# Optimization experiments

Measured on AMD Instinct MI355X. Metric: run time of the kernel, lower is better.

## Reference

```python
import jax, jax.numpy as jnp
import numpy as np
from jax import lax

DIM = 192
HEADS = 6
WIDTH = 256
HEIGHT = 128
BATCH = 2


def _conv1x1(x, w):
    # x: [b,c,h,w], w: [o,c] (1x1 conv, no bias)
    return jnp.einsum('bchw,oc->bohw', x, w)


def setup_inputs() -> dict:
    key = jax.random.key(0)
    ks = jax.random.split(key, 7)
    c = DIM
    std = c ** -0.5
    x = jax.random.normal(ks[0], (BATCH, c, HEIGHT, WIDTH), dtype=jnp.float32)
    rpb_table = 0.02 * jax.random.normal(ks[1], (2 * WIDTH - 1, HEADS), dtype=jnp.float32)
    w_qkv = std * jax.random.normal(ks[2], (3 * c, c), dtype=jnp.float32)
    w_depth = (1.0 / 3.0) * jax.random.normal(ks[3], (3 * c, 1, 3, 3), dtype=jnp.float32)
    w_pre = std * jax.random.normal(ks[4], (c, c), dtype=jnp.float32)
    w_out = std * jax.random.normal(ks[5], (c, c), dtype=jnp.float32)
    w_gate = std * jax.random.normal(ks[6], (c, c), dtype=jnp.float32)
    return {"x": x, "rpb_table": rpb_table, "w_qkv": w_qkv, "w_depth": w_depth,
            "w_pre": w_pre, "w_out": w_out, "w_gate": w_gate, "num_heads": HEADS}


def reference(x, rpb_table, w_qkv, w_depth, w_pre, w_out, w_gate, num_heads):
    b, c, h, w = x.shape
    hd = c // num_heads
    scale = hd ** -0.5

    x_gate = jax.nn.silu(_conv1x1(x, w_gate))

    t = _conv1x1(x, w_qkv)  # [b, 3c, h, w]
    qkv = lax.conv_general_dilated(
        t, w_depth, window_strides=(1, 1), padding='SAME',
        feature_group_count=3 * c,
        dimension_numbers=('NCHW', 'OIHW', 'NCHW'))
    q, k, v = jnp.split(qkv, 3, axis=1)

    def _rows(z):
        # 'b (head c) h w -> b h head w c'
        return z.reshape(b, num_heads, hd, h, w).transpose(0, 3, 1, 4, 2)

    q = _rows(q) * scale
    k = _rows(k)
    v = _rows(v)

    attn = jnp.einsum('bhnic,bhnjc->bhnij', q, k)  # [b, h, heads, w, w]

    # relative position bias: index[i, j] = i - j + (w - 1)
    idx = jnp.arange(w)[:, None] - jnp.arange(w)[None, :] + (w - 1)
    bias = rpb_table[idx].transpose(2, 0, 1)  # [heads, w, w]
    attn = jax.nn.softmax(attn + bias[None, None], axis=-1)

    out = jnp.einsum('bhnij,bhnjc->bhnic', attn, v)
    # 'b h head w c -> b (head c) h w'
    out = out.transpose(0, 2, 4, 1, 3).reshape(b, c, h, w)

    out = _conv1x1(out, w_pre) * x_gate
    return _conv1x1(out, w_out)
```

## Files before the change

kernel.cpp:

```cpp
#include <hip/hip_runtime.h>
#include <hip/hip_bf16.h>
#include <math.h>

#define BATCH 2
#define C 192
#define H 128
#define W 256
#define HEADS 6
#define HD 32
#define HW (H * W)
#define C3 (3 * C)
#define NPX (BATCH * HW)

typedef unsigned short ushort_t;
using bf16x8 = __attribute__((ext_vector_type(8))) short;
using f32x4  = __attribute__((ext_vector_type(4))) float;

static __device__ __forceinline__ float bfbits2f(ushort_t u) {
    return __uint_as_float(((unsigned)u) << 16);
}
static __device__ __forceinline__ ushort_t f2bfbits(float f) {
    __hip_bfloat16 h = __float2bfloat16(f);
    return *reinterpret_cast<ushort_t*>(&h);
}

__global__ __launch_bounds__(256) void prep_w_kernel(
    const float* __restrict__ wq, const float* __restrict__ wg,
    const float* __restrict__ wp, const float* __restrict__ wo,
    ushort_t* __restrict__ dst)
{
    const int i = blockIdx.x * 256 + threadIdx.x;
    const float* src; int off, base;
    if (i < 27648)      { src = wq; off = i;         base = 0; }
    else if (i < 36864) { src = wg; off = i - 27648; base = 110592; }
    else if (i < 46080) { src = wp; off = i - 36864; base = 147456; }
    else                { src = wo; off = i - 46080; base = 184320; }
    float4 v = ((const float4*)src)[off];
    if (i < 9216) {
        const float sc = 0.25503488f;
        v.x *= sc; v.y *= sc; v.z *= sc; v.w *= sc;
    }
    ushort4 o;
    o.x = f2bfbits(v.x); o.y = f2bfbits(v.y);
    o.z = f2bfbits(v.z); o.w = f2bfbits(v.w);
    *(ushort4*)(dst + base + off * 4) = o;
}

__global__ __launch_bounds__(256) void transpose_x_kernel(
    const float* __restrict__ x, ushort_t* __restrict__ xt)
{
    __shared__ uint Xs[64 * 97];
    const int p0 = blockIdx.x * 64;
    const int b  = p0 >> 15, hw0 = p0 & (HW - 1);
    const int t  = threadIdx.x;

    {
        const int px = t & 63, g = t >> 6;
        const float* xb = x + (size_t)b * C * HW + hw0 + px;
#pragma unroll
        for (int i = 0; i < 24; ++i) {
            const int cp = g + i * 4;
            const float v0 = xb[(size_t)(2 * cp) * HW];
            const float v1 = xb[(size_t)(2 * cp + 1) * HW];
            Xs[px * 97 + cp] = (uint)f2bfbits(v0) | ((uint)f2bfbits(v1) << 16);
        }
    }
    __syncthreads();
    {
        const int px = t >> 2, grp = t & 3;
        uint* dst = (uint*)(xt + (size_t)(p0 + px) * C) + grp * 24;
        const uint* s = &Xs[px * 97 + grp * 24];
#pragma unroll
        for (int i = 0; i < 6; ++i) {
            uint4 u;
            u.x = s[i * 4 + 0]; u.y = s[i * 4 + 1];
            u.z = s[i * 4 + 2]; u.w = s[i * 4 + 3];
            *(uint4*)(dst + i * 4) = u;
        }
    }
}

template <int MODE, int OUTKIND, int MT>
__global__ __launch_bounds__(256, 2) void conv_mfma_kernel(
    const ushort_t* __restrict__ in_t, const ushort_t* __restrict__ w_bf,
    void* __restrict__ outp, ushort_t* __restrict__ gate, int ostride)
{
    const int lin = blockIdx.x;
    const int xcd = lin & 7;
    const int jj  = lin >> 3;
    const int pin = jj / MT;
    const int m   = jj - pin * MT;
    const int m0  = m * 64;
    const int p0  = (xcd * 32 + pin) * 256;

    const int t  = threadIdx.x;
    const int wv = t >> 6, lane = t & 63, quad = lane >> 4, l16 = lane & 15;

    __shared__ ushort_t smem[18432];
    ushort_t* As = smem;

    const ushort_t* bp = in_t + (size_t)(p0 + wv * 64 + l16) * C + quad * 8;
    bf16x8 bF[6][4];
#pragma unroll
    for (int ks = 0; ks < 6; ++ks)
#pragma unroll
        for (int ct = 0; ct < 4; ++ct)
            bF[ks][ct] = *(const bf16x8*)(bp + (size_t)(ct * 16) * C + ks * 32);

    {
        const int row = t >> 2, cg = (t & 3) * 48;
        const ushort_t* src = w_bf + (size_t)(m0 + row) * C + cg;
        ushort_t* dst = &As[row * 200 + cg];
#pragma unroll
        for (int i = 0; i < 6; ++i)
            *(bf16x8*)(dst + i * 8) = *(const bf16x8*)(src + i * 8);
    }
    __syncthreads();

    f32x4 acc[4][4];
#pragma unroll
    for (int rt = 0; rt < 4; ++rt)
#pragma unroll
        for (int ct = 0; ct < 4; ++ct) acc[rt][ct] = f32x4{0.f, 0.f, 0.f, 0.f};

#pragma unroll
    for (int ks = 0; ks < 6; ++ks) {
        bf16x8 aF[4];
#pragma unroll
        for (int rt = 0; rt < 4; ++rt)
            aF[rt] = *(const bf16x8*)&As[(rt * 16 + l16) * 200 + quad * 8 + ks * 32];
#pragma unroll
        for (int rt = 0; rt < 4; ++rt)
#pragma unroll
            for (int ct = 0; ct < 4; ++ct)
                acc[rt][ct] = __builtin_amdgcn_mfma_f32_16x16x32_bf16(
                    aF[rt], bF[ks][ct], acc[rt][ct], 0, 0, 0);
    }

    const bool isg = (MODE == 3) && (m >= 9);
    if (MODE == 1 || isg) {
#pragma unroll
        for (int rt = 0; rt < 4; ++rt)
#pragma unroll
            for (int ct = 0; ct < 4; ++ct) {
                f32x4 v = acc[rt][ct];
#pragma unroll
                for (int r = 0; r < 4; ++r)
                    v[r] = v[r] / (1.f + __expf(-v[r]));
                acc[rt][ct] = v;
            }
    }

    if constexpr (OUTKIND == 0) {
        __syncthreads();
        ushort_t* Ls = smem;
#pragma unroll
        for (int rt = 0; rt < 4; ++rt)
#pragma unroll
            for (int ct = 0; ct < 4; ++ct) {
                const f32x4 v = acc[rt][ct];
                ushort4 o;
                o.x = f2bfbits(v[0]); o.y = f2bfbits(v[1]);
                o.z = f2bfbits(v[2]); o.w = f2bfbits(v[3]);
                *(ushort4*)&Ls[(wv * 64 + ct * 16 + l16) * 72 +
                               rt * 16 + quad * 4] = o;
            }
        __syncthreads();

        ushort_t* ob; int osr, chb;
        if constexpr (MODE == 3) {
            ob  = isg ? gate : (ushort_t*)outp;
            osr = isg ? C : C3;
            chb = isg ? m0 - C3 : m0;
        } else {
            ob = (ushort_t*)outp; osr = ostride; chb = m0;
        }
        const int pxl = t >> 3, c8 = (t & 7) * 8;
#pragma unroll
        for (int r = 0; r < 8; ++r) {
            const int px = r * 32 + pxl;
            const bf16x8 v = *(const bf16x8*)&Ls[px * 72 + c8];
            *(bf16x8*)(ob + (size_t)(p0 + px) * osr + chb + c8) = v;
        }
    } else {
        const int bb = p0 >> 15;
        const int hwb = (p0 & (HW - 1)) + wv * 64;
        float* ob = (float*)outp + ((size_t)bb * C + m0) * HW + hwb;
#pragma unroll
        for (int rt = 0; rt < 4; ++rt)
#pragma unroll
            for (int ct = 0; ct < 4; ++ct) {
                const f32x4 v = acc[rt][ct];
#pragma unroll
                for (int r = 0; r < 4; ++r)
                    ob[(size_t)(rt * 16 + quad * 4 + r) * HW + ct * 16 + l16] = v[r];
            }
    }
}

__global__ __launch_bounds__(256) void dwconv3x3_px_kernel(
    const ushort_t* __restrict__ tin, const float* __restrict__ wd,
    ushort_t* __restrict__ out)
{
    __shared__ float wloc[576];
    __shared__ ushort_t Ld[128 * 72];
    const int bx = blockIdx.x;
    const int px_blk = (bx & 7) * 64 + (63 - (bx >> 3));
    const int cb  = blockIdx.y;
    const int tid = threadIdx.x;
    if (tid < 144)
        *(float4*)&wloc[tid * 4] = *(const float4*)(wd + cb * 576 + tid * 4);
    __syncthreads();

    const int chloc = (tid & 7) * 8;
    const int pxl0 = (tid >> 3) * 4;
    const int px = px_blk * 128 + pxl0;
    const int x0 = px & (W - 1);
    const int y  = (px >> 8) & (H - 1);

    const ushort_t* tb = tin + (size_t)px * C3 + cb * 64 + chloc;

    float acc[4][8];
#pragma unroll
    for (int i = 0; i < 4; ++i)
#pragma unroll
        for (int k = 0; k < 8; ++k) acc[i][k] = 0.f;

#pragma unroll
    for (int dy = -1; dy <= 1; ++dy) {
        const int yy = y + dy;
        if (yy < 0 || yy >= H) continue;
        const ushort_t* rp = tb + (ptrdiff_t)dy * W * C3;

        float f[6][8];
#pragma unroll
        for (int d = 0; d < 6; ++d) {
            const int xx = x0 + d - 1;
            if (xx < 0 || xx >= W) {
#pragma unroll
                for (int k = 0; k < 8; ++k) f[d][k] = 0.f;
            } else {
                const bf16x8 v = *(const bf16x8*)(rp + (ptrdiff_t)(d - 1) * C3);
#pragma unroll
                for (int k = 0; k < 8; ++k) f[d][k] = bfbits2f((ushort_t)v[k]);
            }
        }
#pragma unroll
        for (int k = 0; k < 8; ++k) {
            const float* wk = &wloc[(chloc + k) * 9 + (dy + 1) * 3];
            const float w0 = wk[0], w1 = wk[1], w2 = wk[2];
#pragma unroll
            for (int i = 0; i < 4; ++i)
                acc[i][k] += f[i][k] * w0 + f[i + 1][k] * w1 + f[i + 2][k] * w2;
        }
    }

#pragma unroll
    for (int i = 0; i < 4; ++i) {
        bf16x8 o;
#pragma unroll
        for (int k = 0; k < 8; ++k) o[k] = (short)f2bfbits(acc[i][k]);
        *(bf16x8*)&Ld[(pxl0 + i) * 72 + chloc] = o;
    }
    __syncthreads();

    const int pxl = tid >> 3, c8 = (tid & 7) * 8;
#pragma unroll
    for (int r = 0; r < 4; ++r) {
        const int p = r * 32 + pxl;
        const bf16x8 v = *(const bf16x8*)&Ld[p * 72 + c8];
        *(bf16x8*)(out + (size_t)(px_blk * 128 + p) * C3 + cb * 64 + c8) = v;
    }
}

__global__ __launch_bounds__(256, 4) void attention_mfma_kernel(
    const ushort_t* __restrict__ qkv, const float* __restrict__ rpb,
    ushort_t* __restrict__ att)
{
    const int lin  = blockIdx.x;
    const int xcd  = lin & 7;
    const int j    = lin >> 3;
    const int b    = xcd >> 2;
    const int y    = (xcd & 3) * 32 + (j & 31);
    const int head = j >> 5;
    const int t    = threadIdx.x;
    const int wv   = t >> 6;
    const int lane = t & 63;
    const int quad = lane >> 4;
    const int l16  = lane & 15;

    __shared__ __align__(16) char smem[39424];
    ushort_t* Vt = (ushort_t*)smem;
    ushort_t* Pb = (ushort_t*)(smem + 16896);
    ushort_t* rb = (ushort_t*)(smem + 37376);
    float*    Ol = (float*)smem;

    const size_t rowbase = ((size_t)b * HW + (size_t)y * W) * C3;
    const ushort_t* qbase = qkv + rowbase + head * HD + quad * 8;
    const ushort_t* kbase = qbase + C;

    {
        const ushort_t* rowp = qkv + rowbase + (size_t)t * C3 + head * HD;
        bf16x8 vfr[4];
#pragma unroll
        for (int g = 0; g < 4; ++g)
            vfr[g] = *(const bf16x8*)(rowp + 2 * C + g * 8);
#pragma unroll
        for (int g = 0; g < 4; ++g)
#pragma unroll
            for (int k = 0; k < 8; ++k)
                Vt[(g * 8 + k) * 264 + t] = (ushort_t)vfr[g][k];
    }
    {
        const float LOG2E = 1.4426950408889634f;
#pragma unroll
        for (int s2 = 0; s2 < 2; ++s2)
#pragma unroll
            for (int pp = 0; pp < 2; ++pp) {
                const int k = pp * 256 + t;
                const int src = k + s2;
                rb[s2 * 512 + k] =
                    f2bfbits(src <= 510 ? rpb[src * HEADS + head] * LOG2E : 0.f);
            }
    }

    bf16x8 aQ[4];
#pragma unroll
    for (int rt = 0; rt < 4; ++rt)
        aQ[rt] = *(const bf16x8*)(qbase + (size_t)(wv * 64 + rt * 16 + l16) * C3);
    bf16x8 bK = *(const bf16x8*)(kbase + (size_t)l16 * C3);

    __syncthreads();

    ushort_t* PbW = Pb + wv * 2560;
    float lsum[4] = {0.f, 0.f, 0.f, 0.f};
    f32x4 o_acc[4][2];
#pragma unroll
    for (int rt = 0; rt < 4; ++rt)
#pragma unroll
        for (int ct = 0; ct < 2; ++ct)
            o_acc[rt][ct] = f32x4{0.f, 0.f, 0.f, 0.f};

    const int ibase = wv * 64 + l16 + 255 - quad * 4;

    for (int c2 = 0; c2 < 8; ++c2) {
#pragma unroll
        for (int half = 0; half < 2; ++half) {
            const int n  = c2 * 2 + half;
            const int nn = (n < 15) ? n + 1 : 15;
            const bf16x8 bKn =
                *(const bf16x8*)(kbase + (size_t)(nn * 16 + l16) * C3);
#pragma unroll
            for (int rt = 0; rt < 4; ++rt) {
                const int a  = ibase + rt * 16 - n * 16 - 3;
                const int s2 = a & 1;
                const uint* tp = (const uint*)(rb + s2 * 512 + (a - s2));
                const uint u0 = tp[0], u1 = tp[1];
                f32x4 s;
                s[0] = __uint_as_float(u1 & 0xffff0000u);
                s[1] = __uint_as_float(u1 << 16);
                s[2] = __uint_as_float(u0 & 0xffff0000u);
                s[3] = __uint_as_float(u0 << 16);
                s = __builtin_amdgcn_mfma_f32_16x16x32_bf16(bK, aQ[rt], s, 0, 0, 0);
                const float p0 = __builtin_amdgcn_exp2f(s[0]);
                const float p1 = __builtin_amdgcn_exp2f(s[1]);
                const float p2 = __builtin_amdgcn_exp2f(s[2]);
                const float p3 = __builtin_amdgcn_exp2f(s[3]);
                lsum[rt] += (p0 + p1) + (p2 + p3);
                uint2 dd;
                dd.x = (uint)f2bfbits(p0) | ((uint)f2bfbits(p1) << 16);
                dd.y = (uint)f2bfbits(p2) | ((uint)f2bfbits(p3) << 16);
                *(uint2*)&PbW[(rt * 16 + l16) * 40 + half * 16 + quad * 4] = dd;
            }
            bK = bKn;
        }
#pragma unroll
        for (int rt = 0; rt < 4; ++rt) {
            const bf16x8 aP = *(const bf16x8*)&PbW[(rt * 16 + l16) * 40 + quad * 8];
#pragma unroll
            for (int ct = 0; ct < 2; ++ct) {
                const bf16x8 bV = *(const bf16x8*)
                    &Vt[(ct * 16 + l16) * 264 + c2 * 32 + quad * 8];
                o_acc[rt][ct] = __builtin_amdgcn_mfma_f32_16x16x32_bf16(
                    aP, bV, o_acc[rt][ct], 0, 0, 0);
            }
        }
    }

    float linv[4];
#pragma unroll
    for (int rt = 0; rt < 4; ++rt) {
        float v = lsum[rt];
        v += __shfl_xor(v, 16);
        v += __shfl_xor(v, 32);
        linv[rt] = 1.f / v;
    }

    __syncthreads();
#pragma unroll
    for (int rt = 0; rt < 4; ++rt) {
        const int i = wv * 64 + rt * 16 + quad * 4;
        float sc[4];
#pragma unroll
        for (int reg = 0; reg < 4; ++reg)
            sc[reg] = __shfl(linv[rt], quad * 4 + reg);
#pragma unroll
        for (int ct = 0; ct < 2; ++ct) {
            const int c = ct * 16 + l16;
#pragma unroll
            for (int reg = 0; reg < 4; ++reg)
                Ol[c * 257 + i + reg] = o_acc[rt][ct][reg] * sc[reg];
        }
    }
    __syncthreads();

    const size_t orow = (size_t)b * HW + (size_t)y * W;
    const int pxl = t >> 2, part = t & 3;
#pragma unroll
    for (int r = 0; r < 4; ++r) {
        const int px = r * 64 + pxl;
        bf16x8 o;
#pragma unroll
        for (int k = 0; k < 8; ++k)
            o[k] = (short)f2bfbits(Ol[(part * 8 + k) * 257 + px]);
        *(bf16x8*)(att + (orow + px) * C + head * HD + part * 8) = o;
    }
}

__global__ __launch_bounds__(256, 3) void conv2_fused_kernel(
    const ushort_t* __restrict__ att_t, const ushort_t* __restrict__ gatep,
    const ushort_t* __restrict__ wpre, const ushort_t* __restrict__ wout,
    float* __restrict__ outp)
{
    const int lin = blockIdx.x;
    const int xcd = lin & 7;
    const int pin = lin >> 3;
    const int p0  = (xcd * 64 + pin) * 128;

    const int t  = threadIdx.x;
    const int wv = t >> 6, lane = t & 63, quad = lane >> 4, l16 = lane & 15;

    __shared__ ushort_t Zs[4][32 * 200];
    ushort_t* Zw = Zs[wv];
    const int pxw = p0 + wv * 32;

#pragma unroll
    for (int ms = 0; ms < 3; ++ms) {
        f32x4 acc[4][2];
#pragma unroll
        for (int rt = 0; rt < 4; ++rt)
#pragma unroll
            for (int ct = 0; ct < 2; ++ct) acc[rt][ct] = f32x4{0.f,0.f,0.f,0.f};

        const ushort_t* ap = wpre + (size_t)(ms * 64 + l16) * C + quad * 8;
        const ushort_t* bp = att_t + (size_t)(pxw + l16) * C + quad * 8;
#pragma unroll
        for (int ks = 0; ks < 6; ++ks) {
            bf16x8 aF[4];
#pragma unroll
            for (int rt = 0; rt < 4; ++rt)
                aF[rt] = *(const bf16x8*)(ap + (size_t)(rt * 16) * C + ks * 32);
            const bf16x8 b0 = *(const bf16x8*)(bp + ks * 32);
            const bf16x8 b1 = *(const bf16x8*)(bp + (size_t)16 * C + ks * 32);
#pragma unroll
            for (int rt = 0; rt < 4; ++rt) {
                acc[rt][0] = __builtin_amdgcn_mfma_f32_16x16x32_bf16(
                    aF[rt], b0, acc[rt][0], 0, 0, 0);
                acc[rt][1] = __builtin_amdgcn_mfma_f32_16x16x32_bf16(
                    aF[rt], b1, acc[rt][1], 0, 0, 0);
            }
        }
#pragma unroll
        for (int rt = 0; rt < 4; ++rt)
#pragma unroll
            for (int ct = 0; ct < 2; ++ct) {
                const int px = pxw + ct * 16 + l16;
                const int ch = ms * 64 + rt * 16 + quad * 4;
                const ushort4 g = *(const ushort4*)(gatep + (size_t)px * C + ch);
                f32x4 v = acc[rt][ct];
                v[0] *= bfbits2f(g.x); v[1] *= bfbits2f(g.y);
                v[2] *= bfbits2f(g.z); v[3] *= bfbits2f(g.w);
                ushort4 o;
                o.x = f2bfbits(v[0]); o.y = f2bfbits(v[1]);
                o.z = f2bfbits(v[2]); o.w = f2bfbits(v[3]);
                *(ushort4*)&Zw[(ct * 16 + l16) * 200 + ch] = o;
            }
    }

    const int bb  = p0 >> 15;
    const int hwb = (p0 & (HW - 1)) + wv * 32;
#pragma unroll
    for (int ms = 0; ms < 3; ++ms) {
        f32x4 acc[4][2];
#pragma unroll
        for (int rt = 0; rt < 4; ++rt)
#pragma unroll
            for (int ct = 0; ct < 2; ++ct) acc[rt][ct] = f32x4{0.f,0.f,0.f,0.f};

        const ushort_t* ap = wout + (size_t)(ms * 64 + l16) * C + quad * 8;
#pragma unroll
        for (int ks = 0; ks < 6; ++ks) {
            bf16x8 aF[4];
#pragma unroll
            for (int rt = 0; rt < 4; ++rt)
                aF[rt] = *(const bf16x8*)(ap + (size_t)(rt * 16) * C + ks * 32);
            const bf16x8 b0 = *(const bf16x8*)&Zw[l16 * 200 + quad * 8 + ks * 32];
            const bf16x8 b1 = *(const bf16x8*)&Zw[(16 + l16) * 200 + quad * 8 + ks * 32];
#pragma unroll
            for (int rt = 0; rt < 4; ++rt) {
                acc[rt][0] = __builtin_amdgcn_mfma_f32_16x16x32_bf16(
                    aF[rt], b0, acc[rt][0], 0, 0, 0);
                acc[rt][1] = __builtin_amdgcn_mfma_f32_16x16x32_bf16(
                    aF[rt], b1, acc[rt][1], 0, 0, 0);
            }
        }
        float* ob = outp + ((size_t)bb * C + ms * 64) * HW + hwb;
#pragma unroll
        for (int rt = 0; rt < 4; ++rt)
#pragma unroll
            for (int ct = 0; ct < 2; ++ct) {
                const f32x4 v = acc[rt][ct];
#pragma unroll
                for (int r = 0; r < 4; ++r)
                    __builtin_nontemporal_store(v[r],
                        &ob[(size_t)(rt * 16 + quad * 4 + r) * HW + ct * 16 + l16]);
            }
    }
}

extern "C" void kernel_launch(void* const* d_in, const int* in_sizes, int n_in,
                              void* d_out, int out_size, void* d_ws, size_t ws_size,
                              hipStream_t stream)
{
    const float* x       = (const float*)d_in[0];
    const float* rpb     = (const float*)d_in[1];
    const float* w_qkv   = (const float*)d_in[2];
    const float* w_depth = (const float*)d_in[3];
    const float* w_pre   = (const float*)d_in[4];
    const float* w_out   = (const float*)d_in[5];
    const float* w_gate  = (const float*)d_in[6];
    float* out = (float*)d_out;

    char* wsb = (char*)d_ws;
    ushort_t* wbf      = (ushort_t*)wsb;
    ushort_t* w_pre_b  = wbf + 147456;
    ushort_t* w_out_b  = wbf + 184320;
    ushort_t* gate_t   = (ushort_t*)(wsb + 524288u);
    ushort_t* buf_t    = (ushort_t*)(wsb + 25690112u);
    ushort_t* att_t    = (ushort_t*)(wsb + 25690112u);
    ushort_t* buf_qkv  = (ushort_t*)(wsb + 101187584u);
    ushort_t* x_t      = (ushort_t*)(wsb + 101187584u);

    dim3 blk(256);

    prep_w_kernel<<<dim3(216), blk, 0, stream>>>(w_qkv, w_gate, w_pre, w_out, wbf);
    transpose_x_kernel<<<dim3(NPX / 64), blk, 0, stream>>>(x, x_t);
    conv_mfma_kernel<3, 0, 12><<<dim3(3072), blk, 0, stream>>>(
        x_t, wbf, buf_t, gate_t, C3);
    dwconv3x3_px_kernel<<<dim3(NPX / 128, 9), blk, 0, stream>>>(
        buf_t, w_depth, buf_qkv);
    attention_mfma_kernel<<<dim3(H * HEADS * BATCH), blk, 0, stream>>>(
        buf_qkv, rpb, att_t);
    conv2_fused_kernel<<<dim3(NPX / 128), blk, 0, stream>>>(
        att_t, gate_t, w_pre_b, w_out_b, out);
}
```

Baseline: 285.6 us.

## Halve conv2 pixel tile per wave and raise occupancy bounds across conv kernels

The fused pre/out 1x1 conv kernel now has each wave handle 16 pixels instead of 32, and the grid doubles to compensate. The attention B-fragments are preloaded into registers, and the shared-memory row stride changes from 200 to 204. Launch bounds rise to 4 blocks per CU for the QKV conv, depthwise conv and fused conv kernels, trading register headroom for more resident waves. The risks are that each weight fragment is now reused across fewer pixels, so weight traffic from cache doubles, and that the tighter register limits could cause spilling.

Result: slower. 331.6 us (+16.1%).

```diff
diff --git a/kernel.cpp b/kernel.cpp
--- a/kernel.cpp
+++ b/kernel.cpp
@@ -81,7 +81,7 @@
 }
 
 template <int MODE, int OUTKIND, int MT>
-__global__ __launch_bounds__(256, 2) void conv_mfma_kernel(
+__global__ __launch_bounds__(256, 4) void conv_mfma_kernel(
     const ushort_t* __restrict__ in_t, const ushort_t* __restrict__ w_bf,
     void* __restrict__ outp, ushort_t* __restrict__ gate, int ostride)
 {
@@ -198,7 +198,7 @@
     }
 }
 
-__global__ __launch_bounds__(256) void dwconv3x3_px_kernel(
+__global__ __launch_bounds__(256, 4) void dwconv3x3_px_kernel(
     const ushort_t* __restrict__ tin, const float* __restrict__ wd,
     ushort_t* __restrict__ out)
 {
@@ -427,7 +427,7 @@
     }
 }
 
-__global__ __launch_bounds__(256, 3) void conv2_fused_kernel(
+__global__ __launch_bounds__(256, 4) void conv2_fused_kernel(
     const ushort_t* __restrict__ att_t, const ushort_t* __restrict__ gatep,
     const ushort_t* __restrict__ wpre, const ushort_t* __restrict__ wout,
     float* __restrict__ outp)
@@ -435,96 +435,97 @@
     const int lin = blockIdx.x;
     const int xcd = lin & 7;
     const int pin = lin >> 3;
-    const int p0  = (xcd * 64 + pin) * 128;
+    const int p0  = xcd * 8192 + pin * 64;
 
     const int t  = threadIdx.x;
     const int wv = t >> 6, lane = t & 63, quad = lane >> 4, l16 = lane & 15;
 
-    __shared__ ushort_t Zs[4][32 * 200];
+    __shared__ ushort_t Zs[4][16 * 204];
     ushort_t* Zw = Zs[wv];
-    const int pxw = p0 + wv * 32;
+    const int pxw = p0 + wv * 16;
+
+    const ushort_t* bp = att_t + (size_t)(pxw + l16) * C + quad * 8;
+    bf16x8 bB[6];
+#pragma unroll
+    for (int ks = 0; ks < 6; ++ks)
+        bB[ks] = *(const bf16x8*)(bp + ks * 32);
 
 #pragma unroll
     for (int ms = 0; ms < 3; ++ms) {
-        f32x4 acc[4][2];
-#pragma unroll
-        for (int rt = 0; rt < 4; ++rt)
-#pragma unroll
-            for (int ct = 0; ct < 2; ++ct) acc[rt][ct] = f32x4{0.f,0.f,0.f,0.f};
+        f32x4 acc[4];
+#pragma unroll
+        for (int rt = 0; rt < 4; ++rt) acc[rt] = f32x4{0.f,0.f,0.f,0.f};
 
         const ushort_t* ap = wpre + (size_t)(ms * 64 + l16) * C + quad * 8;
-        const ushort_t* bp = att_t + (size_t)(pxw + l16) * C + quad * 8;
-#pragma unroll
-        for (int ks = 0; ks < 6; ++ks) {
-            bf16x8 aF[4];
-#pragma unroll
-            for (int rt = 0; rt < 4; ++rt)
-                aF[rt] = *(const bf16x8*)(ap + (size_t)(rt * 16) * C + ks * 32);
-            const bf16x8 b0 = *(const bf16x8*)(bp + ks * 32);
-            const bf16x8 b1 = *(const bf16x8*)(bp + (size_t)16 * C + ks * 32);
-#pragma unroll
-            for (int rt = 0; rt < 4; ++rt) {
-                acc[rt][0] = __builtin_amdgcn_mfma_f32_16x16x32_bf16(
-                    aF[rt], b0, acc[rt][0], 0, 0, 0);
-                acc[rt][1] = __builtin_amdgcn_mfma_f32_16x16x32_bf16(
-                    aF[rt], b1, acc[rt][1], 0, 0, 0);
-            }
-        }
-#pragma unroll
-        for (int rt = 0; rt < 4; ++rt)
-#pragma unroll
-            for (int ct = 0; ct < 2; ++ct) {
-                const int px = pxw + ct * 16 + l16;
-                const int ch = ms * 64 + rt * 16 + quad * 4;
-                const ushort4 g = *(const ushort4*)(gatep + (size_t)px * C + ch);
-                f32x4 v = acc[rt][ct];
-                v[0] *= bfbits2f(g.x); v[1] *= bfbits2f(g.y);
-                v[2] *= bfbits2f(g.z); v[3] *= bfbits2f(g.w);
-                ushort4 o;
-                o.x = f2bfbits(v[0]); o.y = f2bfbits(v[1]);
-                o.z = f2bfbits(v[2]); o.w = f2bfbits(v[3]);
-                *(ushort4*)&Zw[(ct * 16 + l16) * 200 + ch] = o;
-            }
+#pragma unroll
+        for (int h = 0; h < 2; ++h) {
+            bf16x8 aF[3][4];
+#pragma unroll
+            for (int k2 = 0; k2 < 3; ++k2)
+#pragma unroll
+                for (int rt = 0; rt < 4; ++rt)
+                    aF[k2][rt] = *(const bf16x8*)(ap + (size_t)(rt * 16) * C +
+                                                  (h * 3 + k2) * 32);
+#pragma unroll
+            for (int k2 = 0; k2 < 3; ++k2)
+#pragma unroll
+                for (int rt = 0; rt < 4; ++rt)
+                    acc[rt] = __builtin_amdgcn_mfma_f32_16x16x32_bf16(
+                        aF[k2][rt], bB[h * 3 + k2], acc[rt], 0, 0, 0);
+        }
+
+#pragma unroll
+        for (int rt = 0; rt < 4; ++rt) {
+            const int px = pxw + l16;
+            const int ch = ms * 64 + rt * 16 + quad * 4;
+            const ushort4 g = *(const ushort4*)(gatep + (size_t)px * C + ch);
+            f32x4 v = acc[rt];
+            v[0] *= bfbits2f(g.x); v[1] *= bfbits2f(g.y);
+            v[2] *= bfbits2f(g.z); v[3] *= bfbits2f(g.w);
+            ushort4 o;
+            o.x = f2bfbits(v[0]); o.y = f2bfbits(v[1]);
+            o.z = f2bfbits(v[2]); o.w = f2bfbits(v[3]);
+            *(ushort4*)&Zw[l16 * 204 + ch] = o;
+        }
     }
 
     const int bb  = p0 >> 15;
-    const int hwb = (p0 & (HW - 1)) + wv * 32;
+    const int hwb = (p0 & (HW - 1)) + wv * 16;
 #pragma unroll
     for (int ms = 0; ms < 3; ++ms) {
-        f32x4 acc[4][2];
-#pragma unroll
-        for (int rt = 0; rt < 4; ++rt)
-#pragma unroll
-            for (int ct = 0; ct < 2; ++ct) acc[rt][ct] = f32x4{0.f,0.f,0.f,0.f};
+        f32x4 acc[4];
+#pragma unroll
+        for (int rt = 0; rt < 4; ++rt) acc[rt] = f32x4{0.f,0.f,0.f,0.f};
 
         const ushort_t* ap = wout + (size_t)(ms * 64 + l16) * C + quad * 8;
 #pragma unroll
-        for (int ks = 0; ks < 6; ++ks) {
-            bf16x8 aF[4];
-#pragma unroll
-            for (int rt = 0; rt < 4; ++rt)
-                aF[rt] = *(const bf16x8*)(ap + (size_t)(rt * 16) * C + ks * 32);
-            const bf16x8 b0 = *(const bf16x8*)&Zw[l16 * 200 + quad * 8 + ks * 32];
-            const bf16x8 b1 = *(const bf16x8*)&Zw[(16 + l16) * 200 + quad * 8 + ks * 32];
-#pragma unroll
-            for (int rt = 0; rt < 4; ++rt) {
-                acc[rt][0] = __builtin_amdgcn_mfma_f32_16x16x32_bf16(
-                    aF[rt], b0, acc[rt][0], 0, 0, 0);
-                acc[rt][1] = __builtin_amdgcn_mfma_f32_16x16x32_bf16(
-                    aF[rt], b1, acc[rt][1], 0, 0, 0);
+        for (int h = 0; h < 2; ++h) {
+            bf16x8 aF[3][4];
+#pragma unroll
+            for (int k2 = 0; k2 < 3; ++k2)
+#pragma unroll
+                for (int rt = 0; rt < 4; ++rt)
+                    aF[k2][rt] = *(const bf16x8*)(ap + (size_t)(rt * 16) * C +
+                                                  (h * 3 + k2) * 32);
+#pragma unroll
+            for (int k2 = 0; k2 < 3; ++k2) {
+                const int ks = h * 3 + k2;
+                const bf16x8 b0 = *(const bf16x8*)&Zw[l16 * 204 + quad * 8 + ks * 32];
+#pragma unroll
+                for (int rt = 0; rt < 4; ++rt)
+                    acc[rt] = __builtin_amdgcn_mfma_f32_16x16x32_bf16(
+                        aF[k2][rt], b0, acc[rt], 0, 0, 0);
             }
         }
         float* ob = outp + ((size_t)bb * C + ms * 64) * HW + hwb;
 #pragma unroll
-        for (int rt = 0; rt < 4; ++rt)
-#pragma unroll
-            for (int ct = 0; ct < 2; ++ct) {
-                const f32x4 v = acc[rt][ct];
-#pragma unroll
-                for (int r = 0; r < 4; ++r)
-                    __builtin_nontemporal_store(v[r],
-                        &ob[(size_t)(rt * 16 + quad * 4 + r) * HW + ct * 16 + l16]);
-            }
+        for (int rt = 0; rt < 4; ++rt) {
+            const f32x4 v = acc[rt];
+#pragma unroll
+            for (int r = 0; r < 4; ++r)
+                __builtin_nontemporal_store(v[r],
+                    &ob[(size_t)(rt * 16 + quad * 4 + r) * HW + l16]);
+        }
     }
 }
 
@@ -561,6 +562,6 @@
         buf_t, w_depth, buf_qkv);
     attention_mfma_kernel<<<dim3(H * HEADS * BATCH), blk, 0, stream>>>(
         buf_qkv, rpb, att_t);
-    conv2_fused_kernel<<<dim3(NPX / 128), blk, 0, stream>>>(
+    conv2_fused_kernel<<<dim3(NPX / 64), blk, 0, stream>>>(
         att_t, gate_t, w_pre_b, w_out_b, out);
 }
```
